# Kernel optimization log

Measured on AMD Instinct MI355X. Metric: run time of the kernel, lower is better.

The kernel has to match this reference:

```python
import jax, jax.numpy as jnp
import numpy as np

B, T, D = 4, 2048, 1024
H, K, V, S, C = 8, 128, 128, 512, 256
R = T // C
W = 2 * C
TAU = float(K) ** 0.5
NEG = 1e30  # INFTY_APPROX from source


def rel_shift(x):
    # Transformer-XL relative shift; x: [B,H,R,C,W]
    lead = x.shape[:-2]
    c, w = x.shape[-2:]
    x = jnp.pad(x, [(0, 0)] * (x.ndim - 1) + [(1, 0)])
    x = x.reshape(*lead, w + 1, c)
    return x[..., 1:, :].reshape(*lead, c, w)


def setup_inputs():
    key = jax.random.key(0)
    ks = jax.random.split(key, 9)
    sd = lambda n: 1.0 / np.sqrt(n)
    f32 = jnp.float32
    return dict(
        x=jax.random.normal(ks[0], (B, T, D), f32),
        g_ln=jnp.ones((D,), f32),
        Wq=jax.random.normal(ks[1], (D, H, K), f32) * sd(D),
        Wk=jax.random.normal(ks[2], (D, H, K), f32) * sd(D),
        Wv=jax.random.normal(ks[3], (D, H, V), f32) * sd(D),
        codebook=jax.random.normal(ks[4], (H, S, K), f32),
        xl_r=jax.random.normal(ks[5], (H, W, K), f32) * sd(D),
        xl_u=jax.random.normal(ks[6], (H, K), f32) * 0.02,
        xl_v=jax.random.normal(ks[7], (H, K), f32) * 0.02,
        Wo=jax.random.normal(ks[8], (H, V, D), f32) * sd(H * V),
    )


def reference(x, g_ln, Wq, Wk, Wv, codebook, xl_r, xl_u, xl_v, Wo):
    # RMSNorm
    xt = x * jax.lax.rsqrt(jnp.mean(jnp.square(x), axis=-1, keepdims=True) + 1e-6) * g_ln
    # QKV projections, reshaped to blocks: [B,H,R,C,*]
    q = jnp.einsum('btd,dhk->bhtk', xt, Wq).reshape(B, H, R, C, K)
    k = jnp.einsum('btd,dhk->bhtk', xt, Wk).reshape(B, H, R, C, K)
    v = jnp.einsum('btd,dhv->bhtv', xt, Wv).reshape(B, H, R, C, V)
    # VQ codebook assignment (per-head nearest codeword)
    d2 = (jnp.sum(k * k, -1, keepdims=True)
          - 2.0 * jnp.einsum('bhrck,hsk->bhrcs', k, codebook)
          + jnp.sum(codebook * codebook, -1)[None, :, None, None, :])
    z = jnp.argmin(d2, axis=-1)                      # shortcodes [B,H,R,C]
    delta = jax.nn.one_hot(z, S, dtype=k.dtype)      # [B,H,R,C,S]
    k_hat_q = jnp.einsum('bhrcs,hsk->bhrck', delta, codebook)
    k_hat = k + jax.lax.stop_gradient(k_hat_q - k)   # straight-through quantized keys
    # causal cumulative per-code cluster stats ('matmul' reduction from source)
    d1 = jnp.sum(delta, axis=3)                      # counts per block [B,H,R,S]
    d1c = jnp.cumsum(d1, axis=2)
    fracs = jnp.tril(jnp.einsum('bhrs,bhgs->bhsrg', 1.0 / jnp.clip(d1c, 1.0), d1))
    lower = jnp.pad(d1c[:, :, :-2], ((0, 0), (0, 0), (2, 0), (0, 0)))
    dv = jnp.einsum('bhrcs,bhrcv->bhrsv', delta, v)
    dvn = dv / jnp.clip(d1[..., None], 1.0)
    dvnc = jnp.einsum('bhsrg,bhgsv->bhrsv', fracs, dvn)
    upper_div_lower = jnp.pad(dvnc[:, :, :-2], ((0, 0), (0, 0), (2, 0), (0, 0), (0, 0)))
    # attention over recent window (prev+current block) and codebook cache
    q_u = q + xl_u[None, :, None, None, :]
    q_v = q + xl_v[None, :, None, None, :]
    k_hat_prev = jnp.pad(k_hat[:, :, :-1], ((0, 0), (0, 0), (1, 0), (0, 0), (0, 0)))
    v_prev = jnp.pad(v[:, :, :-1], ((0, 0), (0, 0), (1, 0), (0, 0), (0, 0)))
    k_recent = jnp.concatenate([k_hat_prev, k_hat], axis=3)  # [B,H,R,W,K]
    v_recent = jnp.concatenate([v_prev, v], axis=3)          # [B,H,R,W,V]
    ac = jnp.einsum('bhrck,bhrwk->bhrcw', q_u, k_recent)
    bd = rel_shift(jnp.einsum('bhrck,hwk->bhrcw', q_v, xl_r))
    recent = (ac + bd) / TAU
    i = jnp.arange(C)[:, None]
    j = jnp.arange(W)[None, :]
    causal = j <= i + C                                            # [C,W]
    first = (jnp.arange(R)[:, None, None] == 0) & (j[None] < C)    # mask zero-padded prev of block 0
    mask = causal[None] & jnp.logical_not(first)                   # [R,C,W]
    recent = jnp.where(mask[None, None], recent, -NEG)
    cache = jnp.einsum('bhrck,hsk->bhrcs', q_u, codebook) / TAU
    cache = cache + jnp.where(lower > 0, jnp.log(jnp.maximum(lower, 1.0)), -NEG)[:, :, :, None, :]
    attn = jax.nn.softmax(jnp.concatenate([cache, recent], axis=-1), axis=-1)
    out = (jnp.einsum('bhrcs,bhrsv->bhrcv', attn[..., :S], upper_div_lower)
           + jnp.einsum('bhrcw,bhrwv->bhrcv', attn[..., S:], v_recent))
    res = jnp.einsum('bhtv,hvd->btd', out.reshape(B, H, T, V), Wo)
    return res
```

## Files before the change

kernel.cpp:

```cpp
#include <hip/hip_runtime.h>
#include <hip/hip_fp16.h>

typedef _Float16 half8 __attribute__((ext_vector_type(8)));
typedef float f32x4 __attribute__((ext_vector_type(4)));

constexpr int Bn = 4, Tn = 2048, Dn = 1024, Hn = 8, Kn = 128, Vn = 128;
constexpr int Sn = 512, Cn = 256, Rn = 8, Wn = 512;
constexpr float NEGV = 1.0e30f;
constexpr float INV_TAU = 0.08838834764831845f;

__device__ __forceinline__ half8 ldh8(const __half* p) {
  return *reinterpret_cast<const half8*>(p);
}
__device__ __forceinline__ void sth8(__half* p, half8 v) {
  *reinterpret_cast<half8*>(p) = v;
}
__device__ __forceinline__ f32x4 mfma16(half8 a, half8 b, f32x4 c) {
  return __builtin_amdgcn_mfma_f32_16x16x32_f16(a, b, c, 0, 0, 0);
}

__global__ __launch_bounds__(256) void rms3_k(const float* __restrict__ x,
                                              const float* __restrict__ g,
                                              __half* __restrict__ xth,
                                              __half* __restrict__ xtl) {
  const int row = blockIdx.x;
  const int tid = threadIdx.x;
  const float4 v = reinterpret_cast<const float4*>(x + (size_t)row * Dn)[tid];
  float ss = v.x * v.x + v.y * v.y + v.z * v.z + v.w * v.w;
#pragma unroll
  for (int o = 32; o > 0; o >>= 1) ss += __shfl_xor(ss, o);
  __shared__ float red[4];
  if ((tid & 63) == 0) red[tid >> 6] = ss;
  __syncthreads();
  const float tot = red[0] + red[1] + red[2] + red[3];
  const float sc = rsqrtf(tot * (1.0f / Dn) + 1e-6f);
  const float4 gv = reinterpret_cast<const float4*>(g)[tid];
  float vv[4] = {v.x * sc * gv.x, v.y * sc * gv.y, v.z * sc * gv.z,
                 v.w * sc * gv.w};
  __half hi[4], lo[4];
#pragma unroll
  for (int e = 0; e < 4; ++e) {
    hi[e] = __float2half(vv[e]);
    lo[e] = __float2half(vv[e] - __half2float(hi[e]));
  }
  __half2* oph = reinterpret_cast<__half2*>(xth + (size_t)row * Dn + tid * 4);
  __half2* opl = reinterpret_cast<__half2*>(xtl + (size_t)row * Dn + tid * 4);
  oph[0] = __halves2half2(hi[0], hi[1]);
  oph[1] = __halves2half2(hi[2], hi[3]);
  opl[0] = __halves2half2(lo[0], lo[1]);
  opl[1] = __halves2half2(lo[2], lo[3]);
}

__global__ __launch_bounds__(256) void transcvt_k(const float* __restrict__ src,
                                                  __half* __restrict__ dst) {
  __shared__ float ts[32][33];
  const int bx = blockIdx.x, by = blockIdx.y;
  const int j = threadIdx.x & 31, i0 = threadIdx.x >> 5;
#pragma unroll
  for (int rr = 0; rr < 4; ++rr) {
    const int row = i0 + rr * 8;
    ts[row][j] = src[(size_t)(by * 32 + row) * 1024 + bx * 32 + j];
  }
  __syncthreads();
#pragma unroll
  for (int rr = 0; rr < 4; ++rr) {
    const int row = i0 + rr * 8;
    dst[(size_t)(bx * 32 + row) * 1024 + by * 32 + j] = __float2half(ts[j][row]);
  }
}

__global__ __launch_bounds__(256) void transcvt2_k(
    const float* __restrict__ src, __half* __restrict__ dh,
    __half* __restrict__ dl) {
  __shared__ float ts[32][33];
  const int bx = blockIdx.x, by = blockIdx.y;
  const int j = threadIdx.x & 31, i0 = threadIdx.x >> 5;
#pragma unroll
  for (int rr = 0; rr < 4; ++rr) {
    const int row = i0 + rr * 8;
    ts[row][j] = src[(size_t)(by * 32 + row) * 1024 + bx * 32 + j];
  }
  __syncthreads();
#pragma unroll
  for (int rr = 0; rr < 4; ++rr) {
    const int row = i0 + rr * 8;
    const float v = ts[j][row];
    const __half hi = __float2half(v);
    dh[(size_t)(bx * 32 + row) * 1024 + by * 32 + j] = hi;
    dl[(size_t)(bx * 32 + row) * 1024 + by * 32 + j] =
        __float2half(v - __half2float(hi));
  }
}

__global__ __launch_bounds__(256) void cb2_k(const float* __restrict__ cb,
                                             float* __restrict__ cb2v) {
  const int idx = blockIdx.x * 256 + threadIdx.x;
  const float4* rp = reinterpret_cast<const float4*>(cb + (size_t)idx * Kn);
  float ss = 0.f;
#pragma unroll 8
  for (int i = 0; i < Kn / 4; ++i) {
    const float4 v = rp[i];
    ss += v.x * v.x + v.y * v.y + v.z * v.z + v.w * v.w;
  }
  cb2v[idx] = ss;
}

__global__ __launch_bounds__(256) void cvt2_k(const float* __restrict__ cb,
                                              const float* __restrict__ xlr,
                                              __half* __restrict__ cbh,
                                              __half* __restrict__ cbl,
                                              __half* __restrict__ xlrh) {
  const int i = blockIdx.x * 256 + threadIdx.x;
  constexpr int NE = Hn * Sn * Kn;
  if (i < NE) {
    const float v = cb[i];
    const __half hi = __float2half(v);
    cbh[i] = hi;
    cbl[i] = __float2half(v - __half2float(hi));
  } else {
    xlrh[i - NE] = __float2half(xlr[i - NE]);
  }
}

__global__ __launch_bounds__(256) void duv_k(const float* __restrict__ xlr,
                                             const float* __restrict__ xlu,
                                             const float* __restrict__ xlv,
                                             float* __restrict__ duv) {
  const int h = blockIdx.x;
  const float* up = xlu + h * Kn;
  const float* vp = xlv + h * Kn;
  for (int j = threadIdx.x; j < Wn; j += 256) {
    const float* rp = xlr + ((size_t)h * Wn + j) * Kn;
    float s = 0.f;
#pragma unroll 8
    for (int d = 0; d < Kn; ++d) s = fmaf(vp[d] - up[d], rp[d], s);
    duv[h * Wn + j] = s;
  }
}

__global__ __launch_bounds__(256, 2) void kproj_k(
    const __half* __restrict__ Ah, const __half* __restrict__ Al,
    const __half* __restrict__ Bh, const __half* __restrict__ Bl,
    __half* __restrict__ Ch, __half* __restrict__ Cl, int M, int KD) {
  __shared__ __half AsH[128 * 72];
  __shared__ __half AsL[128 * 72];
  __shared__ __half BsH[128 * 72];
  __shared__ __half BsL[128 * 72];
  const int tid = threadIdx.x;
  const int lane = tid & 63, wq = tid >> 6;
  const int lrow = lane & 15, lk8 = (lane >> 4) << 3;
  const int m0 = blockIdx.x * 128, n0 = blockIdx.y * 128;
  const int srow = tid >> 2, spart = tid & 3;

  f32x4 acc[2][8];
#pragma unroll
  for (int mt = 0; mt < 2; ++mt)
#pragma unroll
    for (int nt = 0; nt < 8; ++nt) acc[mt][nt] = (f32x4){0.f, 0.f, 0.f, 0.f};

  for (int kt = 0; kt < KD; kt += 64) {
    __syncthreads();
#pragma unroll
    for (int hh = 0; hh < 2; ++hh) {
      const int row = srow + hh * 64;
      const size_t ao = (size_t)(m0 + row) * KD + kt + spart * 16;
      const size_t bo = (size_t)(n0 + row) * KD + kt + spart * 16;
      sth8(&AsH[row * 72 + spart * 16], ldh8(Ah + ao));
      sth8(&AsH[row * 72 + spart * 16 + 8], ldh8(Ah + ao + 8));
      sth8(&AsL[row * 72 + spart * 16], ldh8(Al + ao));
      sth8(&AsL[row * 72 + spart * 16 + 8], ldh8(Al + ao + 8));
      sth8(&BsH[row * 72 + spart * 16], ldh8(Bh + bo));
      sth8(&BsH[row * 72 + spart * 16 + 8], ldh8(Bh + bo + 8));
      sth8(&BsL[row * 72 + spart * 16], ldh8(Bl + bo));
      sth8(&BsL[row * 72 + spart * 16 + 8], ldh8(Bl + bo + 8));
    }
    __syncthreads();
#pragma unroll
    for (int ks = 0; ks < 2; ++ks) {
      const half8 a0h = ldh8(&AsH[(32 * wq + lrow) * 72 + lk8 + 32 * ks]);
      const half8 a1h = ldh8(&AsH[(32 * wq + 16 + lrow) * 72 + lk8 + 32 * ks]);
      const half8 a0l = ldh8(&AsL[(32 * wq + lrow) * 72 + lk8 + 32 * ks]);
      const half8 a1l = ldh8(&AsL[(32 * wq + 16 + lrow) * 72 + lk8 + 32 * ks]);
#pragma unroll
      for (int nt = 0; nt < 8; ++nt) {
        const half8 bh = ldh8(&BsH[(16 * nt + lrow) * 72 + lk8 + 32 * ks]);
        const half8 bl = ldh8(&BsL[(16 * nt + lrow) * 72 + lk8 + 32 * ks]);
        acc[0][nt] = mfma16(a0h, bh, acc[0][nt]);
        acc[0][nt] = mfma16(a0h, bl, acc[0][nt]);
        acc[0][nt] = mfma16(a0l, bh, acc[0][nt]);
        acc[1][nt] = mfma16(a1h, bh, acc[1][nt]);
        acc[1][nt] = mfma16(a1h, bl, acc[1][nt]);
        acc[1][nt] = mfma16(a1l, bh, acc[1][nt]);
      }
    }
  }
  __half* OH = Ch + (size_t)(n0 >> 7) * M * 128;
  __half* OL = Cl + (size_t)(n0 >> 7) * M * 128;
#pragma unroll
  for (int mt = 0; mt < 2; ++mt)
#pragma unroll
    for (int nt = 0; nt < 8; ++nt)
#pragma unroll
      for (int reg = 0; reg < 4; ++reg) {
        const int row = m0 + 32 * wq + 16 * mt + 4 * (lane >> 4) + reg;
        const float v = acc[mt][nt][reg];
        const __half hi = __float2half(v);
        OH[(size_t)row * 128 + 16 * nt + lrow] = hi;
        OL[(size_t)row * 128 + 16 * nt + lrow] =
            __float2half(v - __half2float(hi));
      }
}

template <int MODE>
__global__ __launch_bounds__(256, 4) void gemmh_k(const __half* __restrict__ A,
                                                  const __half* __restrict__ Bt,
                                                  void* __restrict__ Cout,
                                                  int M, int N, int KD) {
  __shared__ __half As[128 * 72];
  __shared__ __half Bs[128 * 72];
  const int tid = threadIdx.x;
  const int lane = tid & 63, wq = tid >> 6;
  const int lrow = lane & 15, lk8 = (lane >> 4) << 3;
  const int m0 = blockIdx.x * 128, n0 = blockIdx.y * 128;
  const int srow = tid >> 2, spart = tid & 3;

  f32x4 acc[2][8];
#pragma unroll
  for (int mt = 0; mt < 2; ++mt)
#pragma unroll
    for (int nt = 0; nt < 8; ++nt) acc[mt][nt] = (f32x4){0.f, 0.f, 0.f, 0.f};

  for (int kt = 0; kt < KD; kt += 64) {
    __syncthreads();
#pragma unroll
    for (int hh = 0; hh < 2; ++hh) {
      const int row = srow + hh * 64;
      const __half* pa = A + (size_t)(m0 + row) * KD + kt + spart * 16;
      const __half* pb = Bt + (size_t)(n0 + row) * KD + kt + spart * 16;
      sth8(&As[row * 72 + spart * 16], ldh8(pa));
      sth8(&As[row * 72 + spart * 16 + 8], ldh8(pa + 8));
      sth8(&Bs[row * 72 + spart * 16], ldh8(pb));
      sth8(&Bs[row * 72 + spart * 16 + 8], ldh8(pb + 8));
    }
    __syncthreads();
#pragma unroll
    for (int ks = 0; ks < 2; ++ks) {
      half8 a0 = ldh8(&As[(32 * wq + lrow) * 72 + lk8 + 32 * ks]);
      half8 a1 = ldh8(&As[(32 * wq + 16 + lrow) * 72 + lk8 + 32 * ks]);
#pragma unroll
      for (int nt = 0; nt < 8; ++nt) {
        half8 b = ldh8(&Bs[(16 * nt + lrow) * 72 + lk8 + 32 * ks]);
        acc[0][nt] = mfma16(a0, b, acc[0][nt]);
        acc[1][nt] = mfma16(a1, b, acc[1][nt]);
      }
    }
  }
  if (MODE == 0) {
    __half* O = reinterpret_cast<__half*>(Cout) + (size_t)(n0 >> 7) * M * 128;
#pragma unroll
    for (int mt = 0; mt < 2; ++mt)
#pragma unroll
      for (int nt = 0; nt < 8; ++nt)
#pragma unroll
        for (int reg = 0; reg < 4; ++reg) {
          const int row = m0 + 32 * wq + 16 * mt + 4 * (lane >> 4) + reg;
          O[(size_t)row * 128 + 16 * nt + lrow] = __float2half(acc[mt][nt][reg]);
        }
  } else {
    float* O = reinterpret_cast<float*>(Cout);
#pragma unroll
    for (int mt = 0; mt < 2; ++mt)
#pragma unroll
      for (int nt = 0; nt < 8; ++nt)
#pragma unroll
        for (int reg = 0; reg < 4; ++reg) {
          const int row = m0 + 32 * wq + 16 * mt + 4 * (lane >> 4) + reg;
          O[(size_t)row * N + n0 + 16 * nt + lrow] = acc[mt][nt][reg];
        }
  }
}

__global__ __launch_bounds__(256, 2) void argmin3_k(
    const __half* __restrict__ kbh, const __half* __restrict__ kbl,
    const __half* __restrict__ cbh, const __half* __restrict__ cbl,
    const float* __restrict__ cb2v, int* __restrict__ zb) {
  __shared__ __half BsH[64 * 136];
  __shared__ __half BsL[64 * 136];
  const int tid = threadIdx.x;
  const int lane = tid & 63, wq = tid >> 6;
  const int lrow = lane & 15, lk8 = (lane >> 4) << 3;
  const int m0 = blockIdx.x * 128;
  const int h = blockIdx.y;
  const int srow = tid >> 2, spart = tid & 3;
  const size_t kbase = (size_t)h * (Bn * Tn);

  half8 ah[2][4], al[2][4];
#pragma unroll
  for (int mt = 0; mt < 2; ++mt)
#pragma unroll
    for (int ks = 0; ks < 4; ++ks) {
      const size_t off =
          (kbase + m0 + 32 * wq + 16 * mt + lrow) * 128 + lk8 + 32 * ks;
      ah[mt][ks] = ldh8(kbh + off);
      al[mt][ks] = ldh8(kbl + off);
    }

  float best[2][4];
  int bidx[2][4];
#pragma unroll
  for (int mt = 0; mt < 2; ++mt)
#pragma unroll
    for (int reg = 0; reg < 4; ++reg) {
      best[mt][reg] = 3.0e38f;
      bidx[mt][reg] = 0;
    }

  for (int s0 = 0; s0 < Sn; s0 += 64) {
    __syncthreads();
    {
      const size_t bo = ((size_t)h * Sn + s0 + srow) * 128 + spart * 32;
      sth8(&BsH[srow * 136 + spart * 32], ldh8(cbh + bo));
      sth8(&BsH[srow * 136 + spart * 32 + 8], ldh8(cbh + bo + 8));
      sth8(&BsH[srow * 136 + spart * 32 + 16], ldh8(cbh + bo + 16));
      sth8(&BsH[srow * 136 + spart * 32 + 24], ldh8(cbh + bo + 24));
      sth8(&BsL[srow * 136 + spart * 32], ldh8(cbl + bo));
      sth8(&BsL[srow * 136 + spart * 32 + 8], ldh8(cbl + bo + 8));
      sth8(&BsL[srow * 136 + spart * 32 + 16], ldh8(cbl + bo + 16));
      sth8(&BsL[srow * 136 + spart * 32 + 24], ldh8(cbl + bo + 24));
    }
    __syncthreads();
    f32x4 acc[2][4];
#pragma unroll
    for (int mt = 0; mt < 2; ++mt)
#pragma unroll
      for (int nt = 0; nt < 4; ++nt) acc[mt][nt] = (f32x4){0.f, 0.f, 0.f, 0.f};
#pragma unroll
    for (int ks = 0; ks < 4; ++ks)
#pragma unroll
      for (int nt = 0; nt < 4; ++nt) {
        const half8 bh = ldh8(&BsH[(16 * nt + lrow) * 136 + lk8 + 32 * ks]);
        const half8 bl = ldh8(&BsL[(16 * nt + lrow) * 136 + lk8 + 32 * ks]);
        acc[0][nt] = mfma16(ah[0][ks], bh, acc[0][nt]);
        acc[0][nt] = mfma16(ah[0][ks], bl, acc[0][nt]);
        acc[0][nt] = mfma16(al[0][ks], bh, acc[0][nt]);
        acc[1][nt] = mfma16(ah[1][ks], bh, acc[1][nt]);
        acc[1][nt] = mfma16(ah[1][ks], bl, acc[1][nt]);
        acc[1][nt] = mfma16(al[1][ks], bh, acc[1][nt]);
      }
#pragma unroll
    for (int mt = 0; mt < 2; ++mt)
#pragma unroll
      for (int nt = 0; nt < 4; ++nt) {
        const int s = s0 + 16 * nt + lrow;
        const float c2 = cb2v[h * Sn + s];
#pragma unroll
        for (int reg = 0; reg < 4; ++reg) {
          const float d2 = c2 - 2.0f * acc[mt][nt][reg];
          if (d2 < best[mt][reg]) {
            best[mt][reg] = d2;
            bidx[mt][reg] = s;
          }
        }
      }
  }
#pragma unroll
  for (int xb = 1; xb <= 8; xb <<= 1) {
#pragma unroll
    for (int mt = 0; mt < 2; ++mt)
#pragma unroll
      for (int reg = 0; reg < 4; ++reg) {
        const float ob = __shfl_xor(best[mt][reg], xb);
        const int oi = __shfl_xor(bidx[mt][reg], xb);
        if (ob < best[mt][reg] ||
            (ob == best[mt][reg] && oi < bidx[mt][reg])) {
          best[mt][reg] = ob;
          bidx[mt][reg] = oi;
        }
      }
  }
  if (lrow == 0) {
#pragma unroll
    for (int mt = 0; mt < 2; ++mt)
#pragma unroll
      for (int reg = 0; reg < 4; ++reg) {
        const int row = m0 + 32 * wq + 16 * mt + 4 * (lane >> 4) + reg;
        zb[kbase + row] = bidx[mt][reg];
      }
  }
}

__global__ __launch_bounds__(1024) void scan2_k(const int* __restrict__ zb,
                                                const __half* __restrict__ vb,
                                                __half* __restrict__ udl,
                                                float* __restrict__ biasv) {
  __shared__ float acc[64][128];
  __shared__ float cnt[64];
  const int tid = threadIdx.x;
  const int sc = blockIdx.x, b = blockIdx.y, h = blockIdx.z;
  const int s0 = sc * 64;
  for (int i = tid; i < 64 * 128; i += 1024) acc[i >> 7][i & 127] = 0.f;
  if (tid < 64) cnt[tid] = 0.f;
  __syncthreads();
  const size_t tokH = (size_t)h * (Bn * Tn) + (size_t)b * Tn;
  const int dd = tid & 127, slice = tid >> 7;
  for (int r = 0; r < Rn; ++r) {
    for (int i = tid; i < 64 * 128; i += 1024) {
      const int srow = i >> 7, d = i & 127;
      const float c = cnt[srow];
      udl[((((size_t)h * Bn + b) * Rn + r) * Sn + s0 + srow) * Vn + d] =
          __float2half(acc[srow][d] / fmaxf(c, 1.f));
    }
    if (tid < 64) {
      const float c = cnt[tid];
      biasv[(((size_t)h * Bn + b) * Rn + r) * Sn + s0 + tid] =
          (c > 0.f) ? logf(c) : -NEGV;
    }
    __syncthreads();
    if (r >= 1 && r < 7) {
      const int tb = (r - 1) * Cn;
#pragma unroll 4
      for (int u = 0; u < 32; ++u) {
        const int tok = tb + u * 8 + slice;
        const int s = zb[tokH + tok];
        if (s >= s0 && s < s0 + 64) {
          const float v = __half2float(vb[(tokH + tok) * Vn + dd]);
          atomicAdd(&acc[s - s0][dd], v);
          if (dd == 0) atomicAdd(&cnt[s - s0], 1.0f);
        }
      }
    }
    __syncthreads();
  }
}

__global__ __launch_bounds__(256, 2) void attn3_k(
    const __half* __restrict__ qbh, const __half* __restrict__ vbh,
    const __half* __restrict__ udl, const __half* __restrict__ cbh,
    const __half* __restrict__ xlrh, const float* __restrict__ biasv,
    const float* __restrict__ duv, const int* __restrict__ zb,
    const float* __restrict__ xlu, __half* __restrict__ aout) {
  __shared__ __half quS[64 * 136];
  __shared__ __half KXS[64 * 136];
  __shared__ __half VtS[128 * 72];
  __shared__ __half PBD[64 * 136];
  __shared__ float duvS[128];
  __shared__ float biasS[64];

  const int tid = threadIdx.x;
  const int lane = tid & 63, wq = tid >> 6;
  const int lrow = lane & 15, lk8 = (lane >> 4) << 3;
  const int qt = blockIdx.x;
  const int b = blockIdx.y >> 3, r = blockIdx.y & 7;
  const int h = blockIdx.z;
  const int c0 = qt * 64;
  const int tBlk = r * Cn + c0;
  const size_t tokH = (size_t)h * (Bn * Tn) + (size_t)b * Tn;
  const size_t sBase = (((size_t)h * Bn + b) * Rn + r) * Sn;
  const int srow = tid >> 2, spart = tid & 3;
  const int kp = tid >> 3, p8 = tid & 7;

  {
    const __half* src = qbh + (tokH + tBlk + srow) * Kn + spart * 32;
    const float* up = xlu + h * Kn + spart * 32;
    alignas(16) __half tmp[32];
#pragma unroll
    for (int e = 0; e < 32; ++e)
      tmp[e] = __float2half(__half2float(src[e]) + up[e]);
#pragma unroll
    for (int g2 = 0; g2 < 4; ++g2)
      sth8(&quS[srow * 136 + spart * 32 + g2 * 8],
           *reinterpret_cast<half8*>(&tmp[g2 * 8]));
  }

  float mR[4], lR[4];
  f32x4 Oacc[8];
#pragma unroll
  for (int i = 0; i < 4; ++i) {
    mR[i] = -NEGV;
    lR[i] = 0.f;
  }
#pragma unroll
  for (int nt = 0; nt < 8; ++nt) Oacc[nt] = (f32x4){0.f, 0.f, 0.f, 0.f};

  half8 a[4];
  bool aLoaded = false;

  for (int ch = 0; ch < 16; ++ch) {
    const bool isC = (ch < 8);
    const int s0 = ch * 64;
    const int w0 = (ch - 8) * 64;
    const int jbase = w0 + 192 - c0;
    __syncthreads();
    if (isC) {
      const __half* ks = cbh + ((size_t)h * Sn + s0 + srow) * Kn + spart * 32;
      sth8(&KXS[srow * 136 + spart * 32], ldh8(ks));
      sth8(&KXS[srow * 136 + spart * 32 + 8], ldh8(ks + 8));
      sth8(&KXS[srow * 136 + spart * 32 + 16], ldh8(ks + 16));
      sth8(&KXS[srow * 136 + spart * 32 + 24], ldh8(ks + 24));
      const __half* u0 = udl + (sBase + s0 + 2 * kp) * Vn + p8 * 16;
      const __half* u1 = u0 + Vn;
#pragma unroll
      for (int e = 0; e < 16; ++e) {
        const int d = p8 * 16 + e;
        const int gidx = ((2 * kp) >> 3) ^ ((d >> 4) & 7);
        *reinterpret_cast<__half2*>(
            &VtS[d * 72 + gidx * 8 + ((2 * kp) & 7)]) =
            __halves2half2(u0[e], u1[e]);
      }
      if (tid < 64) biasS[tid] = biasv[sBase + s0 + tid];
    } else {
      int tk = (r - 1) * Cn + w0 + srow;
      if (tk < 0) tk = 0;
      const int code = zb[tokH + tk];
      const __half* ks = cbh + ((size_t)h * Sn + code) * Kn + spart * 32;
      sth8(&KXS[srow * 136 + spart * 32], ldh8(ks));
      sth8(&KXS[srow * 136 + spart * 32 + 8], ldh8(ks + 8));
      sth8(&KXS[srow * 136 + spart * 32 + 16], ldh8(ks + 16));
      sth8(&KXS[srow * 136 + spart * 32 + 24], ldh8(ks + 24));
      const int tk0 = (r - 1) * Cn + w0 + 2 * kp;
      const int tka = tk0 < 0 ? 0 : tk0;
      const int tkb = tk0 + 1 < 0 ? 0 : tk0 + 1;
      const __half* v0 = vbh + (tokH + tka) * Kn + p8 * 16;
      const __half* v1 = vbh + (tokH + tkb) * Kn + p8 * 16;
#pragma unroll
      for (int e = 0; e < 16; ++e) {
        const int d = p8 * 16 + e;
        const int gidx = ((2 * kp) >> 3) ^ ((d >> 4) & 7);
        *reinterpret_cast<__half2*>(
            &VtS[d * 72 + gidx * 8 + ((2 * kp) & 7)]) =
            __halves2half2(v0[e], v1[e]);
      }
    }
    __syncthreads();
    if (!aLoaded) {
#pragma unroll
      for (int ks = 0; ks < 4; ++ks)
        a[ks] = ldh8(&quS[(16 * wq + lrow) * 136 + lk8 + 32 * ks]);
      aLoaded = true;
    }
    f32x4 acc[4];
#pragma unroll
    for (int nt = 0; nt < 4; ++nt) acc[nt] = (f32x4){0.f, 0.f, 0.f, 0.f};
#pragma unroll
    for (int ks = 0; ks < 4; ++ks)
#pragma unroll
      for (int nt = 0; nt < 4; ++nt)
        acc[nt] = mfma16(
            a[ks], ldh8(&KXS[(16 * nt + lrow) * 136 + lk8 + 32 * ks]),
            acc[nt]);

    float lg[4][4];
    if (isC) {
#pragma unroll
      for (int nt = 0; nt < 4; ++nt) {
        const float bv = biasS[lrow + 16 * nt];
#pragma unroll
        for (int reg = 0; reg < 4; ++reg)
          lg[nt][reg] = acc[nt][reg] * INV_TAU + bv;
      }
    } else {
#pragma unroll
      for (int hh = 0; hh < 2; ++hh) {
        __syncthreads();
        {
          int j = jbase + hh * 64 + srow;
          j = j < 0 ? 0 : (j > Wn - 1 ? Wn - 1 : j);
          const __half* xs = xlrh + ((size_t)h * Wn + j) * Kn + spart * 32;
          sth8(&KXS[srow * 136 + spart * 32], ldh8(xs));
          sth8(&KXS[srow * 136 + spart * 32 + 8], ldh8(xs + 8));
          sth8(&KXS[srow * 136 + spart * 32 + 16], ldh8(xs + 16));
          sth8(&KXS[srow * 136 + spart * 32 + 24], ldh8(xs + 24));
          if (hh == 0 && tid < 128) {
            int jx = jbase + tid;
            jx = jx < 0 ? 0 : (jx > Wn - 1 ? Wn - 1 : jx);
            duvS[tid] = duv[h * Wn + jx];
          }
        }
        __syncthreads();
        f32x4 bdh[4];
#pragma unroll
        for (int nt = 0; nt < 4; ++nt) bdh[nt] = (f32x4){0.f, 0.f, 0.f, 0.f};
#pragma unroll
        for (int ks = 0; ks < 4; ++ks)
#pragma unroll
          for (int nt = 0; nt < 4; ++nt)
            bdh[nt] = mfma16(
                a[ks], ldh8(&KXS[(16 * nt + lrow) * 136 + lk8 + 32 * ks]),
                bdh[nt]);
#pragma unroll
        for (int nt = 0; nt < 4; ++nt) {
          const int col = hh * 64 + 16 * nt + lrow;
          const float dv = duvS[col];
#pragma unroll
          for (int reg = 0; reg < 4; ++reg) {
            const int row64 = 16 * wq + 4 * (lane >> 4) + reg;
            PBD[row64 * 136 + col] = __float2half(bdh[nt][reg] + dv);
          }
        }
      }
      __syncthreads();
#pragma unroll
      for (int nt = 0; nt < 4; ++nt) {
        const int key = lrow + 16 * nt;
        const int w = w0 + key;
#pragma unroll
        for (int reg = 0; reg < 4; ++reg) {
          const int row64 = 16 * wq + 4 * (lane >> 4) + reg;
          const bool valid = (w <= c0 + row64 + Cn) && !(r == 0 && w < Cn);
          const float bdv = __half2float(PBD[row64 * 136 + key + 63 - row64]);
          lg[nt][reg] = valid ? (acc[nt][reg] + bdv) * INV_TAU : -NEGV;
        }
      }
      __syncthreads();
    }
    float p[4][4], scl[4];
#pragma unroll
    for (int reg = 0; reg < 4; ++reg) {
      float rm = fmaxf(fmaxf(lg[0][reg], lg[1][reg]),
                       fmaxf(lg[2][reg], lg[3][reg]));
      rm = fmaxf(rm, __shfl_xor(rm, 1));
      rm = fmaxf(rm, __shfl_xor(rm, 2));
      rm = fmaxf(rm, __shfl_xor(rm, 4));
      rm = fmaxf(rm, __shfl_xor(rm, 8));
      const float mn = fmaxf(mR[reg], rm);
      scl[reg] = __expf(mR[reg] - mn);
      float rs = 0.f;
#pragma unroll
      for (int nt = 0; nt < 4; ++nt) {
        p[nt][reg] = __expf(lg[nt][reg] - mn);
        rs += p[nt][reg];
      }
      rs += __shfl_xor(rs, 1);
      rs += __shfl_xor(rs, 2);
      rs += __shfl_xor(rs, 4);
      rs += __shfl_xor(rs, 8);
      lR[reg] = lR[reg] * scl[reg] + rs;
      mR[reg] = mn;
    }
#pragma unroll
    for (int nt = 0; nt < 8; ++nt)
#pragma unroll
      for (int reg = 0; reg < 4; ++reg) Oacc[nt][reg] *= scl[reg];
#pragma unroll
    for (int nt = 0; nt < 4; ++nt)
#pragma unroll
      for (int reg = 0; reg < 4; ++reg) {
        const int row64 = 16 * wq + 4 * (lane >> 4) + reg;
        PBD[row64 * 136 + lrow + 16 * nt] = __float2half(p[nt][reg]);
      }
    __syncthreads();
#pragma unroll
    for (int ks = 0; ks < 2; ++ks) {
      half8 pa = ldh8(&PBD[(16 * wq + lrow) * 136 + lk8 + 32 * ks]);
#pragma unroll
      for (int nt = 0; nt < 8; ++nt) {
        const int gidx = (((lk8 + 32 * ks) >> 3) ^ nt);
        half8 vb = ldh8(&VtS[(16 * nt + lrow) * 72 + gidx * 8]);
        Oacc[nt] = mfma16(pa, vb, Oacc[nt]);
      }
    }
  }
  float inv[4];
#pragma unroll
  for (int reg = 0; reg < 4; ++reg) inv[reg] = 1.0f / lR[reg];
#pragma unroll
  for (int nt = 0; nt < 8; ++nt)
#pragma unroll
    for (int reg = 0; reg < 4; ++reg) {
      const int row64 = 16 * wq + 4 * (lane >> 4) + reg;
      aout[((size_t)b * Tn + tBlk + row64) * (Hn * Vn) + h * Vn + 16 * nt +
           lrow] = __float2half(Oacc[nt][reg] * inv[reg]);
    }
}

extern "C" void kernel_launch(void* const* d_in, const int* in_sizes, int n_in,
                              void* d_out, int out_size, void* d_ws,
                              size_t ws_size, hipStream_t stream) {
  (void)in_sizes;
  (void)n_in;
  (void)out_size;
  const float* x = (const float*)d_in[0];
  const float* g_ln = (const float*)d_in[1];
  const float* Wq = (const float*)d_in[2];
  const float* Wk = (const float*)d_in[3];
  const float* Wv = (const float*)d_in[4];
  const float* cb = (const float*)d_in[5];
  const float* xl_r = (const float*)d_in[6];
  const float* xl_u = (const float*)d_in[7];
  const float* xl_v = (const float*)d_in[8];
  const float* Wo = (const float*)d_in[9];
  float* out = (float*)d_out;

  float* W = (float*)d_ws;
  size_t o = 0;
  __half* xth = (__half*)(W + o);
  __half* aout = xth;
  o += (size_t)Bn * Tn * Dn / 2;
  __half* xtl = (__half*)(W + o);
  o += (size_t)Bn * Tn * Dn / 2;
  __half* kbh = (__half*)(W + o);
  __half* udlh = kbh;
  o += (size_t)Hn * Bn * Tn * Kn / 2;
  __half* kbl = (__half*)(W + o);
  o += (size_t)Hn * Bn * Tn * Kn / 2;
  __half* qbh = (__half*)(W + o);
  o += (size_t)Hn * Bn * Tn * Kn / 2;
  __half* vbh = (__half*)(W + o);
  o += (size_t)Hn * Bn * Tn * Vn / 2;
  __half* cbh = (__half*)(W + o);
  o += (size_t)Hn * Sn * Kn / 2;
  __half* cbl = (__half*)(W + o);
  o += (size_t)Hn * Sn * Kn / 2;
  __half* xlrh = (__half*)(W + o);
  o += (size_t)Hn * Wn * Kn / 2;
  int* zb = (int*)(W + o);
  o += (size_t)Hn * Bn * Tn;
  float* biasb = W + o;
  o += (size_t)Hn * Bn * Rn * Sn;
  float* duvb = W + o;
  o += (size_t)Hn * Wn;
  float* cb2b = W + o;
  o += (size_t)Hn * Sn;
  __half* wkth = (__half*)(W + o);
  o += (size_t)Dn * Dn / 2;
  __half* wktl = (__half*)(W + o);
  o += (size_t)Dn * Dn / 2;
  __half* wqt = (__half*)(W + o);
  o += (size_t)Dn * Dn / 2;
  __half* wvt = (__half*)(W + o);
  o += (size_t)Dn * Dn / 2;
  __half* wot = (__half*)(W + o);
  o += (size_t)Dn * Dn / 2;

  if (ws_size < o * sizeof(float)) return;

  rms3_k<<<Bn * Tn, 256, 0, stream>>>(x, g_ln, xth, xtl);
  transcvt2_k<<<dim3(32, 32), 256, 0, stream>>>(Wk, wkth, wktl);
  transcvt_k<<<dim3(32, 32), 256, 0, stream>>>(Wq, wqt);
  transcvt_k<<<dim3(32, 32), 256, 0, stream>>>(Wv, wvt);
  transcvt_k<<<dim3(32, 32), 256, 0, stream>>>(Wo, wot);
  cb2_k<<<Hn * Sn / 256, 256, 0, stream>>>(cb, cb2b);
  cvt2_k<<<2 * Hn * Sn * Kn / 256, 256, 0, stream>>>(cb, xl_r, cbh, cbl, xlrh);
  duv_k<<<Hn, 256, 0, stream>>>(xl_r, xl_u, xl_v, duvb);

  kproj_k<<<dim3(64, 8), 256, 0, stream>>>(xth, xtl, wkth, wktl, kbh, kbl,
                                           8192, 1024);
  gemmh_k<0><<<dim3(64, 8), 256, 0, stream>>>(xth, wqt, qbh, 8192, 1024, 1024);
  gemmh_k<0><<<dim3(64, 8), 256, 0, stream>>>(xth, wvt, vbh, 8192, 1024, 1024);

  argmin3_k<<<dim3(Bn * Tn / 128, Hn), 256, 0, stream>>>(kbh, kbl, cbh, cbl,
                                                         cb2b, zb);
  scan2_k<<<dim3(8, Bn, Hn), 1024, 0, stream>>>(zb, vbh, udlh, biasb);

  attn3_k<<<dim3(4, Bn * Rn, Hn), 256, 0, stream>>>(
      qbh, vbh, udlh, cbh, xlrh, biasb, duvb, zb, xl_u, aout);

  gemmh_k<1><<<dim3(64, 8), 256, 0, stream>>>(aout, wot, out, 8192, 1024,
                                              1024);
}
```

Baseline: 434.7 us.

## Restructure attention kernel to 128-row blocks with per-wave relative-position band

The attention kernel now uses 512-thread blocks covering 128 query rows. Codebook and key fragments are read directly from global memory into MFMA operands instead of being staged through shared memory. The relative-position term is computed per wave as a narrow 80-column band (5 tiles instead of 8), and probabilities are kept in a per-wave buffer. This removes several block-wide barriers and shared-memory traffic. In exchange it relies on cache hits for repeated global loads of codebook and xl_r rows, and wider blocks reduce the grid size.

```diff
diff --git a/kernel.cpp b/kernel.cpp
--- a/kernel.cpp
+++ b/kernel.cpp
@@ -433,43 +433,42 @@
   }
 }
 
-__global__ __launch_bounds__(256, 2) void attn3_k(
+__global__ __launch_bounds__(512, 4) void attn4_k(
     const __half* __restrict__ qbh, const __half* __restrict__ vbh,
     const __half* __restrict__ udl, const __half* __restrict__ cbh,
     const __half* __restrict__ xlrh, const float* __restrict__ biasv,
     const float* __restrict__ duv, const int* __restrict__ zb,
     const float* __restrict__ xlu, __half* __restrict__ aout) {
-  __shared__ __half quS[64 * 136];
-  __shared__ __half KXS[64 * 136];
   __shared__ __half VtS[128 * 72];
-  __shared__ __half PBD[64 * 136];
-  __shared__ float duvS[128];
-  __shared__ float biasS[64];
+  __shared__ __half Ubuf[8 * 16 * 80];
+  __shared__ int zsm[64];
 
   const int tid = threadIdx.x;
   const int lane = tid & 63, wq = tid >> 6;
-  const int lrow = lane & 15, lk8 = (lane >> 4) << 3;
+  const int lrow = lane & 15, hi = lane >> 4;
+  const int lk8 = hi << 3;
   const int qt = blockIdx.x;
   const int b = blockIdx.y >> 3, r = blockIdx.y & 7;
   const int h = blockIdx.z;
-  const int c0 = qt * 64;
-  const int tBlk = r * Cn + c0;
+  const int cb0 = 128 * qt + 16 * wq;
   const size_t tokH = (size_t)h * (Bn * Tn) + (size_t)b * Tn;
   const size_t sBase = (((size_t)h * Bn + b) * Rn + r) * Sn;
-  const int srow = tid >> 2, spart = tid & 3;
-  const int kp = tid >> 3, p8 = tid & 7;
-
+  const int tBlk = r * Cn;
+  __half* Ew = &Ubuf[wq * 16 * 80];
+
+  half8 a[4];
   {
-    const __half* src = qbh + (tokH + tBlk + srow) * Kn + spart * 32;
-    const float* up = xlu + h * Kn + spart * 32;
-    alignas(16) __half tmp[32];
-#pragma unroll
-    for (int e = 0; e < 32; ++e)
-      tmp[e] = __float2half(__half2float(src[e]) + up[e]);
-#pragma unroll
-    for (int g2 = 0; g2 < 4; ++g2)
-      sth8(&quS[srow * 136 + spart * 32 + g2 * 8],
-           *reinterpret_cast<half8*>(&tmp[g2 * 8]));
+    const size_t qrow = (tokH + tBlk + cb0 + lrow) * Kn;
+#pragma unroll
+    for (int ks = 0; ks < 4; ++ks) {
+      const int col = lk8 + 32 * ks;
+      half8 q = ldh8(qbh + qrow + col);
+      const float* up = xlu + h * Kn + col;
+      half8 t;
+#pragma unroll
+      for (int e = 0; e < 8; ++e) t[e] = (_Float16)((float)q[e] + up[e]);
+      a[ks] = t;
+    }
   }
 
   float mR[4], lR[4];
@@ -482,136 +481,125 @@
 #pragma unroll
   for (int nt = 0; nt < 8; ++nt) Oacc[nt] = (f32x4){0.f, 0.f, 0.f, 0.f};
 
-  half8 a[4];
-  bool aLoaded = false;
+  const int kp = tid >> 4, p16 = tid & 15;
 
   for (int ch = 0; ch < 16; ++ch) {
     const bool isC = (ch < 8);
     const int s0 = ch * 64;
     const int w0 = (ch - 8) * 64;
-    const int jbase = w0 + 192 - c0;
     __syncthreads();
     if (isC) {
-      const __half* ks = cbh + ((size_t)h * Sn + s0 + srow) * Kn + spart * 32;
-      sth8(&KXS[srow * 136 + spart * 32], ldh8(ks));
-      sth8(&KXS[srow * 136 + spart * 32 + 8], ldh8(ks + 8));
-      sth8(&KXS[srow * 136 + spart * 32 + 16], ldh8(ks + 16));
-      sth8(&KXS[srow * 136 + spart * 32 + 24], ldh8(ks + 24));
-      const __half* u0 = udl + (sBase + s0 + 2 * kp) * Vn + p8 * 16;
+      const __half* u0 = udl + (sBase + s0 + 2 * kp) * Vn + p16 * 8;
       const __half* u1 = u0 + Vn;
 #pragma unroll
-      for (int e = 0; e < 16; ++e) {
-        const int d = p8 * 16 + e;
+      for (int e = 0; e < 8; ++e) {
+        const int d = p16 * 8 + e;
         const int gidx = ((2 * kp) >> 3) ^ ((d >> 4) & 7);
-        *reinterpret_cast<__half2*>(
-            &VtS[d * 72 + gidx * 8 + ((2 * kp) & 7)]) =
+        *reinterpret_cast<__half2*>(&VtS[d * 72 + gidx * 8 + ((2 * kp) & 7)]) =
             __halves2half2(u0[e], u1[e]);
       }
-      if (tid < 64) biasS[tid] = biasv[sBase + s0 + tid];
     } else {
-      int tk = (r - 1) * Cn + w0 + srow;
-      if (tk < 0) tk = 0;
-      const int code = zb[tokH + tk];
-      const __half* ks = cbh + ((size_t)h * Sn + code) * Kn + spart * 32;
-      sth8(&KXS[srow * 136 + spart * 32], ldh8(ks));
-      sth8(&KXS[srow * 136 + spart * 32 + 8], ldh8(ks + 8));
-      sth8(&KXS[srow * 136 + spart * 32 + 16], ldh8(ks + 16));
-      sth8(&KXS[srow * 136 + spart * 32 + 24], ldh8(ks + 24));
-      const int tk0 = (r - 1) * Cn + w0 + 2 * kp;
-      const int tka = tk0 < 0 ? 0 : tk0;
-      const int tkb = tk0 + 1 < 0 ? 0 : tk0 + 1;
-      const __half* v0 = vbh + (tokH + tka) * Kn + p8 * 16;
-      const __half* v1 = vbh + (tokH + tkb) * Kn + p8 * 16;
-#pragma unroll
-      for (int e = 0; e < 16; ++e) {
-        const int d = p8 * 16 + e;
-        const int gidx = ((2 * kp) >> 3) ^ ((d >> 4) & 7);
-        *reinterpret_cast<__half2*>(
-            &VtS[d * 72 + gidx * 8 + ((2 * kp) & 7)]) =
-            __halves2half2(v0[e], v1[e]);
-      }
-    }
-    __syncthreads();
-    if (!aLoaded) {
-#pragma unroll
-      for (int ks = 0; ks < 4; ++ks)
-        a[ks] = ldh8(&quS[(16 * wq + lrow) * 136 + lk8 + 32 * ks]);
-      aLoaded = true;
-    }
+      if (tid < 64) {
+        int tk = (r - 1) * Cn + w0 + tid;
+        if (tk < 0) tk = 0;
+        zsm[tid] = zb[tokH + tk];
+      }
+      {
+        const int tk0 = (r - 1) * Cn + w0 + 2 * kp;
+        const int tka = tk0 < 0 ? 0 : tk0;
+        const int tkb = tk0 + 1 < 0 ? 0 : tk0 + 1;
+        const __half* v0 = vbh + (tokH + tka) * Kn + p16 * 8;
+        const __half* v1 = vbh + (tokH + tkb) * Kn + p16 * 8;
+#pragma unroll
+        for (int e = 0; e < 8; ++e) {
+          const int d = p16 * 8 + e;
+          const int gidx = ((2 * kp) >> 3) ^ ((d >> 4) & 7);
+          *reinterpret_cast<__half2*>(
+              &VtS[d * 72 + gidx * 8 + ((2 * kp) & 7)]) =
+              __halves2half2(v0[e], v1[e]);
+        }
+      }
+      const int jb = w0 + 240 - cb0;
+#pragma unroll
+      for (int half5 = 0; half5 < 2; ++half5) {
+        const int ntn = half5 ? 2 : 3;
+        f32x4 eacc[3];
+#pragma unroll
+        for (int nt = 0; nt < 3; ++nt) eacc[nt] = (f32x4){0.f, 0.f, 0.f, 0.f};
+#pragma unroll
+        for (int ks = 0; ks < 4; ++ks) {
+#pragma unroll
+          for (int nt = 0; nt < 3; ++nt) {
+            if (nt < ntn) {
+              int j = jb + 16 * (nt + 3 * half5) + lrow;
+              j = j < 0 ? 0 : (j > Wn - 1 ? Wn - 1 : j);
+              eacc[nt] = mfma16(
+                  a[ks], ldh8(xlrh + ((size_t)h * Wn + j) * Kn + lk8 + 32 * ks),
+                  eacc[nt]);
+            }
+          }
+        }
+#pragma unroll
+        for (int nt = 0; nt < 3; ++nt) {
+          if (nt < ntn) {
+            int j = jb + 16 * (nt + 3 * half5) + lrow;
+            j = j < 0 ? 0 : (j > Wn - 1 ? Wn - 1 : j);
+            const float dv = duv[h * Wn + j];
+#pragma unroll
+            for (int reg = 0; reg < 4; ++reg) {
+              Ew[(4 * hi + reg) * 80 + 16 * (nt + 3 * half5) + lrow] =
+                  __float2half(eacc[nt][reg] + dv);
+            }
+          }
+        }
+      }
+    }
+    __syncthreads();
+
     f32x4 acc[4];
 #pragma unroll
     for (int nt = 0; nt < 4; ++nt) acc[nt] = (f32x4){0.f, 0.f, 0.f, 0.f};
-#pragma unroll
-    for (int ks = 0; ks < 4; ++ks)
-#pragma unroll
-      for (int nt = 0; nt < 4; ++nt)
-        acc[nt] = mfma16(
-            a[ks], ldh8(&KXS[(16 * nt + lrow) * 136 + lk8 + 32 * ks]),
-            acc[nt]);
-
+    if (isC) {
+#pragma unroll
+      for (int nt = 0; nt < 4; ++nt) {
+        const __half* kr = cbh + ((size_t)h * Sn + s0 + 16 * nt + lrow) * Kn;
+#pragma unroll
+        for (int ks = 0; ks < 4; ++ks)
+          acc[nt] = mfma16(a[ks], ldh8(kr + lk8 + 32 * ks), acc[nt]);
+      }
+    } else {
+#pragma unroll
+      for (int nt = 0; nt < 4; ++nt) {
+        const int code = zsm[16 * nt + lrow];
+        const __half* kr = cbh + ((size_t)h * Sn + code) * Kn;
+#pragma unroll
+        for (int ks = 0; ks < 4; ++ks)
+          acc[nt] = mfma16(a[ks], ldh8(kr + lk8 + 32 * ks), acc[nt]);
+      }
+    }
     float lg[4][4];
     if (isC) {
 #pragma unroll
       for (int nt = 0; nt < 4; ++nt) {
-        const float bv = biasS[lrow + 16 * nt];
+        const float bv = biasv[sBase + s0 + 16 * nt + lrow];
 #pragma unroll
         for (int reg = 0; reg < 4; ++reg)
           lg[nt][reg] = acc[nt][reg] * INV_TAU + bv;
       }
     } else {
 #pragma unroll
-      for (int hh = 0; hh < 2; ++hh) {
-        __syncthreads();
-        {
-          int j = jbase + hh * 64 + srow;
-          j = j < 0 ? 0 : (j > Wn - 1 ? Wn - 1 : j);
-          const __half* xs = xlrh + ((size_t)h * Wn + j) * Kn + spart * 32;
-          sth8(&KXS[srow * 136 + spart * 32], ldh8(xs));
-          sth8(&KXS[srow * 136 + spart * 32 + 8], ldh8(xs + 8));
-          sth8(&KXS[srow * 136 + spart * 32 + 16], ldh8(xs + 16));
-          sth8(&KXS[srow * 136 + spart * 32 + 24], ldh8(xs + 24));
-          if (hh == 0 && tid < 128) {
-            int jx = jbase + tid;
-            jx = jx < 0 ? 0 : (jx > Wn - 1 ? Wn - 1 : jx);
-            duvS[tid] = duv[h * Wn + jx];
-          }
-        }
-        __syncthreads();
-        f32x4 bdh[4];
-#pragma unroll
-        for (int nt = 0; nt < 4; ++nt) bdh[nt] = (f32x4){0.f, 0.f, 0.f, 0.f};
-#pragma unroll
-        for (int ks = 0; ks < 4; ++ks)
-#pragma unroll
-          for (int nt = 0; nt < 4; ++nt)
-            bdh[nt] = mfma16(
-                a[ks], ldh8(&KXS[(16 * nt + lrow) * 136 + lk8 + 32 * ks]),
-                bdh[nt]);
-#pragma unroll
-        for (int nt = 0; nt < 4; ++nt) {
-          const int col = hh * 64 + 16 * nt + lrow;
-          const float dv = duvS[col];
-#pragma unroll
-          for (int reg = 0; reg < 4; ++reg) {
-            const int row64 = 16 * wq + 4 * (lane >> 4) + reg;
-            PBD[row64 * 136 + col] = __float2half(bdh[nt][reg] + dv);
-          }
-        }
-      }
-      __syncthreads();
-#pragma unroll
       for (int nt = 0; nt < 4; ++nt) {
-        const int key = lrow + 16 * nt;
+        const int key = 16 * nt + lrow;
         const int w = w0 + key;
 #pragma unroll
         for (int reg = 0; reg < 4; ++reg) {
-          const int row64 = 16 * wq + 4 * (lane >> 4) + reg;
-          const bool valid = (w <= c0 + row64 + Cn) && !(r == 0 && w < Cn);
-          const float bdv = __half2float(PBD[row64 * 136 + key + 63 - row64]);
+          const int cl = 4 * hi + reg;
+          const int c = cb0 + cl;
+          const bool valid = (w <= c + Cn) && !(r == 0 && w < Cn);
+          const float bdv = __half2float(Ew[cl * 80 + key + 15 - cl]);
           lg[nt][reg] = valid ? (acc[nt][reg] + bdv) * INV_TAU : -NEGV;
         }
       }
-      __syncthreads();
     }
     float p[4][4], scl[4];
 #pragma unroll
@@ -644,19 +632,16 @@
 #pragma unroll
     for (int nt = 0; nt < 4; ++nt)
 #pragma unroll
-      for (int reg = 0; reg < 4; ++reg) {
-        const int row64 = 16 * wq + 4 * (lane >> 4) + reg;
-        PBD[row64 * 136 + lrow + 16 * nt] = __float2half(p[nt][reg]);
-      }
-    __syncthreads();
+      for (int reg = 0; reg < 4; ++reg)
+        Ew[(4 * hi + reg) * 72 + lrow + 16 * nt] = __float2half(p[nt][reg]);
 #pragma unroll
     for (int ks = 0; ks < 2; ++ks) {
-      half8 pa = ldh8(&PBD[(16 * wq + lrow) * 136 + lk8 + 32 * ks]);
+      half8 pa = ldh8(&Ew[lrow * 72 + lk8 + 32 * ks]);
 #pragma unroll
       for (int nt = 0; nt < 8; ++nt) {
         const int gidx = (((lk8 + 32 * ks) >> 3) ^ nt);
-        half8 vb = ldh8(&VtS[(16 * nt + lrow) * 72 + gidx * 8]);
-        Oacc[nt] = mfma16(pa, vb, Oacc[nt]);
+        half8 vv = ldh8(&VtS[(16 * nt + lrow) * 72 + gidx * 8]);
+        Oacc[nt] = mfma16(pa, vv, Oacc[nt]);
       }
     }
   }
@@ -667,9 +652,9 @@
   for (int nt = 0; nt < 8; ++nt)
 #pragma unroll
     for (int reg = 0; reg < 4; ++reg) {
-      const int row64 = 16 * wq + 4 * (lane >> 4) + reg;
-      aout[((size_t)b * Tn + tBlk + row64) * (Hn * Vn) + h * Vn + 16 * nt +
-           lrow] = __float2half(Oacc[nt][reg] * inv[reg]);
+      const int c = cb0 + 4 * hi + reg;
+      aout[((size_t)b * Tn + tBlk + c) * (Hn * Vn) + h * Vn + 16 * nt + lrow] =
+          __float2half(Oacc[nt][reg] * inv[reg]);
     }
 }
 
@@ -752,7 +737,7 @@
                                                          cb2b, zb);
   scan2_k<<<dim3(8, Bn, Hn), 1024, 0, stream>>>(zb, vbh, udlh, biasb);
 
-  attn3_k<<<dim3(4, Bn * Rn, Hn), 256, 0, stream>>>(
+  attn4_k<<<dim3(2, Bn * Rn, Hn), 512, 0, stream>>>(
       qbh, vbh, udlh, cbh, xlrh, biasb, duvb, zb, xl_u, aout);
 
   gemmh_k<1><<<dim3(64, 8), 256, 0, stream>>>(aout, wot, out, 8192, 1024,
```

Measured after the change: 518.2 us. 19.2% more time.
